# Performance work log

Hardware: AMD Instinct MI355X
Metric: run time of the kernel (lower is better)

The kernel has to match this reference:

```python
import jax, jax.numpy as jnp
import numpy as np

COST_CLS, COST_MASK, COST_DICE = 2.0, 5.0, 5.0


def setup_inputs() -> dict:
    key = jax.random.key(0)
    k1, k2, k3, k4 = jax.random.split(key, 4)
    B, Q, C, H, W, T, Hg, Wg = 4, 100, 81, 256, 256, 20, 512, 512
    pred_logits = jax.random.normal(k1, (B, Q, C), dtype=jnp.float32)
    pred_masks = jax.random.normal(k2, (B, Q, H, W), dtype=jnp.float32)
    # binary GT instance masks (original uses 0/1 masks)
    tgt_masks = (jax.random.uniform(k3, (B, T, Hg, Wg)) < 0.5).astype(jnp.float32)
    tgt_labels = jax.random.randint(k4, (B, T), 0, C).astype(jnp.int64)
    return {"pred_logits": pred_logits, "pred_masks": pred_masks,
            "tgt_masks": tgt_masks, "tgt_labels": tgt_labels}


def _cost_matrices(pred_logits, pred_masks, tgt_masks, tgt_labels):
    # pred_logits [B,Q,C], pred_masks [B,Q,H,W], tgt_masks [B,T,Hg,Wg], tgt_labels [B,T]
    B, Q, H, W = pred_masks.shape
    T, Hg, Wg = tgt_masks.shape[1:]
    # F.interpolate(mode='nearest') down to pred mask size: src = floor(dst * in/out)
    ri = (jnp.arange(H) * Hg) // H
    ci = (jnp.arange(W) * Wg) // W
    tgt = tgt_masks[:, :, ri][:, :, :, ci]          # [B,T,H,W]
    pm = pred_masks.reshape(B, Q, H * W)            # [B,Q,HW]
    tm = tgt.reshape(B, T, H * W)                   # [B,T,HW]
    hw = float(H * W)
    # classification cost: -softmax(logits)[:, tgt_ids]
    prob = jax.nn.softmax(pred_logits, axis=-1)     # [B,Q,C]
    cost_class = -jnp.take_along_axis(prob, tgt_labels[:, None, :], axis=2)  # [B,Q,T]
    # batch_sigmoid_ce_loss: mean over pixels of BCE-with-logits vs 0/1 target
    pos = jax.nn.softplus(-pm)                      # -log sigmoid(x)
    neg = jax.nn.softplus(pm)                       # -log (1 - sigmoid(x))
    cost_mask = (jnp.einsum('bqp,btp->bqt', pos, tm)
                 + jnp.einsum('bqp,btp->bqt', neg, 1.0 - tm)) / hw
    # batch_dice_loss
    sig = jax.nn.sigmoid(pm)
    numer = 2.0 * jnp.einsum('bqp,btp->bqt', sig, tm)
    denom = sig.sum(-1)[:, :, None] + tm.sum(-1)[:, None, :]
    cost_dice = 1.0 - (numer + 1.0) / (denom + 1.0)
    C = COST_CLS * cost_class + COST_MASK * cost_mask + COST_DICE * cost_dice
    return jnp.nan_to_num(C, nan=0.0)               # [B,Q,T]


_cost_jit = jax.jit(_cost_matrices)


def _lsa(cost):
    """Shortest-augmenting-path linear sum assignment (scipy algorithm).
    cost: (R, Cn) numpy array with R <= Cn. Returns col4row[r] = assigned column."""
    R, Cn = cost.shape
    u = np.zeros(R, dtype=np.float64)
    v = np.zeros(Cn, dtype=np.float64)
    col4row = np.full(R, -1, dtype=np.int64)
    row4col = np.full(Cn, -1, dtype=np.int64)
    cost = cost.astype(np.float64)
    for cur_row in range(R):
        shortest = np.full(Cn, np.inf)
        path = np.full(Cn, -1, dtype=np.int64)
        SR = np.zeros(R, dtype=bool)
        SC = np.zeros(Cn, dtype=bool)
        i = cur_row
        minVal = 0.0
        sink = -1
        while sink == -1:
            SR[i] = True
            rem = np.where(~SC)[0]
            d = minVal + cost[i, rem] - u[i] - v[rem]
            upd = d < shortest[rem]
            shortest[rem[upd]] = d[upd]
            path[rem[upd]] = i
            jloc = rem[np.argmin(shortest[rem])]
            minVal = shortest[jloc]
            SC[jloc] = True
            if row4col[jloc] == -1:
                sink = jloc
            else:
                i = row4col[jloc]
        u[cur_row] += minVal
        mask = SR.copy(); mask[cur_row] = False
        u[mask] += minVal - shortest[col4row[mask]]
        v[SC] -= minVal - shortest[SC]
        j = sink
        while True:
            i = path[j]
            row4col[j] = i
            col4row[i], j = j, col4row[i]
            if i == cur_row:
                break
    return col4row


def reference(pred_logits, pred_masks, tgt_masks, tgt_labels):
    C = _cost_jit(pred_logits, pred_masks, tgt_masks, tgt_labels)  # [B,Q,T]
    Cn = np.asarray(C)
    B, Q, T = Cn.shape
    pred_idx, tgt_idx = [], []
    for b in range(B):
        # solve on the transpose (T <= Q): target t -> query q[t]
        q = _lsa(Cn[b].T)
        t = np.arange(T)
        order = np.argsort(q)  # scipy returns row (query) indices in sorted order
        pred_idx.append(q[order])
        tgt_idx.append(t[order])
    return (C,
            jnp.asarray(np.stack(pred_idx), dtype=jnp.int64),
            jnp.asarray(np.stack(tgt_idx), dtype=jnp.int64))
```

## Files before the change

### kernel.cpp

```cpp
#include <hip/hip_runtime.h>
#include <hip/hip_bf16.h>
#include <math.h>
#include <stdint.h>

#define NB 4
#define NQ 100
#define NQR 101
#define NCLS 81
#define NT 20
#define NHW 65536

#define SC 256
#define CPX (NHW / SC)
#define TP 32

typedef __attribute__((ext_vector_type(8))) short bf16x8;
typedef __attribute__((ext_vector_type(16))) float f32x16;

__device__ inline short to_bf16(float f) {
    __hip_bfloat16 h = __float2bfloat16(f);
    return __builtin_bit_cast(short, h);
}

__device__ inline float fast_exp2(float x) { return __builtin_amdgcn_exp2f(x); }
__device__ inline float fast_log2(float x) { return __builtin_amdgcn_logf(x); }

__global__ void __launch_bounds__(256)
k_main(const float* __restrict__ pm, const float* __restrict__ tgt,
       float* __restrict__ A_part, float* __restrict__ D_part,
       float* __restrict__ Sp_part) {
    int gid = blockIdx.x;
    int chunk = gid & (SC - 1);
    int b = gid >> 8;
    int tid = threadIdx.x;
    int wv = tid >> 6, lane = tid & 63;
    int p0 = chunk * CPX;

    __shared__ uint32_t s_tb[CPX];
    __shared__ float s_pm[128 * 64];
    __shared__ short s_bf[4][512];

    if (tid < 128) {
        const float* base = tgt + (((size_t)b * NT) * 512 + 2 * chunk) * 512 + 4 * tid;
        uint32_t w0 = 0, w1 = 0;
#pragma unroll
        for (int t = 0; t < NT; ++t) {
            float4 v = *reinterpret_cast<const float4*>(base + (size_t)t * 512 * 512);
            w0 |= (v.x > 0.5f ? 1u : 0u) << t;
            w1 |= (v.z > 0.5f ? 1u : 0u) << t;
        }
        s_tb[2 * tid] = w0;
        s_tb[2 * tid + 1] = w1;
    }
    __syncthreads();

    int r0 = tid >> 4, cw = tid & 15;
    int Rg = wv * 32 + (lane & 31);
    int h = lane >> 5;
    const bool ones_row = (Rg == NQ);
    bf16x8 ones;
#pragma unroll
    for (int e = 0; e < 8; ++e) ones[e] = (short)0x3F80;

    f32x16 accA, accD;
#pragma unroll
    for (int r = 0; r < 16; ++r) { accA[r] = 0.0f; accD[r] = 0.0f; }
    float mxsum = 0.0f, l2sum = 0.0f;
    const float LOG2E = 1.4426950408889634f;

    for (int st = 0; st < 4; ++st) {
        {
            int ls = wv;
            int col = lane & 31;
            int kbase = st * 64 + ls * 16 + (h << 3);
            uint32_t pk[4];
#pragma unroll
            for (int e2 = 0; e2 < 4; ++e2) {
                uint32_t w0 = s_tb[kbase + 2 * e2];
                uint32_t w1 = s_tb[kbase + 2 * e2 + 1];
                uint32_t lo, hi;
                if (col < NT)       { lo = ((w0 >> col) & 1u) ? 0x3F80u : 0u;
                                      hi = ((w1 >> col) & 1u) ? 0x3F80u : 0u; }
                else if (col == NT) { lo = 0x3F80u; hi = 0x3F80u; }
                else                { lo = 0u; hi = 0u; }
                pk[e2] = lo | (hi << 16);
            }
            *reinterpret_cast<uint4*>(&s_bf[ls][lane * 8]) =
                *reinterpret_cast<const uint4*>(pk);
        }
#pragma unroll
        for (int p = 0; p < 8; ++p) {
            int row = r0 + 16 * p;
            float4 v = make_float4(0.0f, 0.0f, 0.0f, 0.0f);
            if (row < NQ)
                v = *reinterpret_cast<const float4*>(
                    pm + ((size_t)(b * NQ + row)) * NHW + (p0 + st * 64 + cw * 4));
            *reinterpret_cast<float4*>(
                &s_pm[row * 64 + ((cw ^ (row & 15)) << 2)]) = v;
        }
        __syncthreads();
#pragma unroll
        for (int sl = 0; sl < 4; ++sl) {
            int c0 = sl * 4 + h * 2;
            float4 xa = *reinterpret_cast<const float4*>(
                &s_pm[Rg * 64 + ((c0 ^ (Rg & 15)) << 2)]);
            float4 xb4 = *reinterpret_cast<const float4*>(
                &s_pm[Rg * 64 + (((c0 + 1) ^ (Rg & 15)) << 2)]);
            float xs[8] = {xa.x, xa.y, xa.z, xa.w, xb4.x, xb4.y, xb4.z, xb4.w};
            bf16x8 af, sf;
#pragma unroll
            for (int e = 0; e < 8; ++e) {
                float xi = xs[e];
                float y = xi * LOG2E;
                float e1 = fast_exp2(0.0f - fabsf(y));
                float tt = 1.0f + e1;
                float inv = __builtin_amdgcn_rcpf(tt);
                float sig = (xi >= 0.0f) ? inv : e1 * inv;
                l2sum += fast_log2(tt);
                mxsum += fmaxf(xi, 0.0f);
                af[e] = to_bf16(xi);
                sf[e] = to_bf16(sig);
            }
            if (ones_row) af = ones;
            bf16x8 bf = *reinterpret_cast<const bf16x8*>(&s_bf[sl][lane * 8]);
            accA = __builtin_amdgcn_mfma_f32_32x32x16_bf16(af, bf, accA, 0, 0, 0);
            accD = __builtin_amdgcn_mfma_f32_32x32x16_bf16(sf, bf, accD, 0, 0, 0);
        }
        __syncthreads();
    }

    int t = lane & 31;
#pragma unroll
    for (int r = 0; r < 16; ++r) {
        int rowD = (r & 3) + 8 * (r >> 2) + 4 * (lane >> 5);
        int qo = wv * 32 + rowD;
        if (qo <= NQ && t <= NT) {
            size_t base = ((size_t)(b * NQR + qo) * SC + chunk) * TP + t;
            A_part[base] = accA[r];
            D_part[base] = accD[r];
        }
    }
    float sp = fmaf(0.6931471805599453f, l2sum, mxsum);
    sp += __shfl_xor(sp, 32);
    if (lane < 32 && Rg < NQ)
        Sp_part[(size_t)(b * NQ + Rg) * SC + chunk] = sp;
}

__global__ void __launch_bounds__(256)
k_assemble(const float* __restrict__ logits, const int* __restrict__ labels,
           const float* __restrict__ A_part, const float* __restrict__ D_part,
           const float* __restrict__ Sp_part, float* __restrict__ Cout) {
    int bq = blockIdx.x;
    int q = bq % NQ, b = bq / NQ;
    int tid = threadIdx.x, wv = tid >> 6, lane = tid & 63;
    int t = tid & 31, g = tid >> 5;
    __shared__ float sA[4][32], sD[4][32], sS[4][32], sSn[4];

    const float* pa = A_part + (size_t)(b * NQR + q) * SC * TP;
    const float* pd = D_part + (size_t)(b * NQR + q) * SC * TP;
    const float* ps = A_part + (size_t)(b * NQR + NQ) * SC * TP;
    const float* pp = Sp_part + (size_t)(b * NQ + q) * SC;

    float a = 0.0f, d = 0.0f, s = 0.0f;
    for (int c = g; c < SC; c += 8) {
        a += pa[c * TP + t];
        d += pd[c * TP + t];
        s += ps[c * TP + t];
    }
    a += __shfl_xor(a, 32);
    d += __shfl_xor(d, 32);
    s += __shfl_xor(s, 32);
    if (lane < 32) { sA[wv][lane] = a; sD[wv][lane] = d; sS[wv][lane] = s; }
    {
        float sp = pp[tid];
        for (int o = 32; o; o >>= 1) sp += __shfl_xor(sp, o);
        if (lane == 0) sSn[wv] = sp;
    }
    __syncthreads();

    if (wv == 0) {
        int lt = (lane < 32) ? lane : 0;
        float At4 = sA[0][lt] + sA[1][lt] + sA[2][lt] + sA[3][lt];
        float Dt4 = sD[0][lt] + sD[1][lt] + sD[2][lt] + sD[3][lt];
        float St4 = sS[0][lt] + sS[1][lt] + sS[2][lt] + sS[3][lt];
        float Sneg = sSn[0] + sSn[1] + sSn[2] + sSn[3];
        float Ssig = __shfl(Dt4, NT);

        const float* lg = logits + (size_t)bq * NCLS;
        float x0 = (lane < NCLS) ? lg[lane] : -INFINITY;
        float x1 = (lane + 64 < NCLS) ? lg[lane + 64] : -INFINITY;
        float mx = fmaxf(x0, x1);
        for (int o = 32; o; o >>= 1) mx = fmaxf(mx, __shfl_xor(mx, o));
        float s0 = (lane < NCLS) ? __expf(x0 - mx) : 0.0f;
        float s1 = (lane + 64 < NCLS) ? __expf(x1 - mx) : 0.0f;
        float sum = s0 + s1;
        for (int o = 32; o; o >>= 1) sum += __shfl_xor(sum, o);

        if (lane < NT) {
            int label = labels[b * NT + lane];
            float prob = __expf(lg[label] - mx) / sum;
            float cm = (Sneg - At4) * (1.0f / (float)NHW);
            float cd = 1.0f - (2.0f * Dt4 + 1.0f) / (Ssig + St4 + 1.0f);
            float c = 2.0f * (-prob) + 5.0f * cm + 5.0f * cd;
            if (isnan(c)) c = 0.0f;
            Cout[(size_t)bq * NT + lane] = c;
        }
    }
}

__global__ void __launch_bounds__(64)
k_lsa(const float* __restrict__ Cmat, float* __restrict__ out) {
    int b = blockIdx.x;
    int lane = threadIdx.x;
    __shared__ double s_cost[NT][128];

    for (int idx = lane; idx < NT * 128; idx += 64) {
        int r = idx >> 7, j = idx & 127;
        s_cost[r][j] = (j < NQ) ? (double)Cmat[((size_t)b * NQ + j) * NT + r] : 0.0;
    }
    __syncthreads();

    int j0 = lane, j1 = lane + 64;
    bool v1ok = (j1 < NQ);
    double v_0 = 0.0, v_1 = 0.0;
    int r4c0 = -1, r4c1 = -1;
    double u_r = 0.0;
    int c4r = -1;

    for (int cur = 0; cur < NT; ++cur) {
        double sh0 = INFINITY, sh1 = INFINITY;
        int p0 = -1, p1 = -1;
        bool sc0 = false, sc1 = false;
        bool SRr = false;
        int i = cur, sink = -1;
        double minVal = 0.0;

        while (true) {
            if (lane == i) SRr = true;
            double ui = __shfl(u_r, i);
            double c0 = s_cost[i][j0];
            double c1 = s_cost[i][j1 & 127];
            if (!sc0) {
                double d = (minVal + c0 - ui) - v_0;
                if (d < sh0) { sh0 = d; p0 = i; }
            }
            if (v1ok && !sc1) {
                double d = (minVal + c1 - ui) - v_1;
                if (d < sh1) { sh1 = d; p1 = i; }
            }
            double cand0 = (!sc0) ? sh0 : INFINITY;
            double cand1 = (v1ok && !sc1) ? sh1 : INFINITY;
            double bv; int bj;
            if (cand0 <= cand1) { bv = cand0; bj = j0; }
            else                { bv = cand1; bj = j1; }
            for (int o = 32; o; o >>= 1) {
                double ov = __shfl_xor(bv, o);
                int oj = __shfl_xor(bj, o);
                if (ov < bv || (ov == bv && oj < bj)) { bv = ov; bj = oj; }
            }
            minVal = bv;
            if (bj < 64) { if (lane == bj) sc0 = true; }
            else         { if (lane == bj - 64) sc1 = true; }
            int r4 = (bj < 64) ? __shfl(r4c0, bj) : __shfl(r4c1, bj - 64);
            if (r4 == -1) { sink = bj; break; }
            i = r4;
        }

        {
            int c = c4r;
            double g0 = __shfl(sh0, c & 63);
            double g1 = __shfl(sh1, (c - 64) & 63);
            double shc = (c < 64) ? g0 : g1;
            if (lane == cur) u_r += minVal;
            else if (lane < NT && SRr) u_r += minVal - shc;
        }
        if (sc0) v_0 -= minVal - sh0;
        if (v1ok && sc1) v_1 -= minVal - sh1;

        int j = sink;
        while (true) {
            int ii = (j < 64) ? __shfl(p0, j) : __shfl(p1, j - 64);
            if (j < 64) { if (lane == j) r4c0 = ii; }
            else        { if (lane == j - 64) r4c1 = ii; }
            int nj = __shfl(c4r, ii);
            if (lane == ii) c4r = j;
            if (ii == cur) break;
            j = nj;
        }
    }

    int my = c4r;
    int rank = 0;
#pragma unroll
    for (int t2 = 0; t2 < NT; ++t2) {
        int vv = __shfl(my, t2);
        rank += (vv < my) ? 1 : 0;
    }
    if (lane < NT) {
        out[NB * NQ * NT + b * NT + rank] = (float)my;
        out[NB * NQ * NT + NB * NT + b * NT + rank] = (float)lane;
    }
}

extern "C" void kernel_launch(void* const* d_in, const int* in_sizes, int n_in,
                              void* d_out, int out_size, void* d_ws, size_t ws_size,
                              hipStream_t stream) {
    const float* pred_logits = (const float*)d_in[0];
    const float* pred_masks  = (const float*)d_in[1];
    const float* tgt_masks   = (const float*)d_in[2];
    const int*   tgt_labels  = (const int*)d_in[3];
    float* out = (float*)d_out;

    char* ws = (char*)d_ws;
    float* A_part  = (float*)ws;
    float* D_part  = A_part + (size_t)NB * NQR * SC * TP;
    float* Sp_part = D_part + (size_t)NB * NQR * SC * TP;

    k_main<<<NB * SC, 256, 0, stream>>>(pred_masks, tgt_masks, A_part, D_part, Sp_part);
    k_assemble<<<NB * NQ, 256, 0, stream>>>(pred_logits, tgt_labels, A_part, D_part,
                                            Sp_part, out);
    k_lsa<<<NB, 64, 0, stream>>>(out, out);
}
```

Measured before the change: 82.17 us.

## Double-buffer pred-mask tiles with async global_load_lds prefetch

Replaces the per-stage synchronous float4 loads of pred mask tiles into LDS with direct global-to-LDS DMA loads (global_load_lds), double-buffered across two LDS banks so stage st+2 is fetched while stage st is computed. The target bf16 operand tile is likewise double-buffered and built one stage ahead. Manual vmcnt/lgkmcnt waits and raw s_barrier replace __syncthreads. The aim is to hide global memory latency behind the MFMA and transcendental work. The cost is more LDS, fragile hand-written wait counts, and rows past NQ now reading past the end of the bank instead of zeros.

```diff
diff --git a/kernel.cpp b/kernel.cpp
--- a/kernel.cpp
+++ b/kernel.cpp
@@ -16,6 +16,8 @@
 
 typedef __attribute__((ext_vector_type(8))) short bf16x8;
 typedef __attribute__((ext_vector_type(16))) float f32x16;
+typedef __attribute__((address_space(1))) const void gvoid_t;
+typedef __attribute__((address_space(3))) void svoid_t;
 
 __device__ inline short to_bf16(float f) {
     __hip_bfloat16 h = __float2bfloat16(f);
@@ -24,6 +26,21 @@
 
 __device__ inline float fast_exp2(float x) { return __builtin_amdgcn_exp2f(x); }
 __device__ inline float fast_log2(float x) { return __builtin_amdgcn_logf(x); }
+
+__device__ inline void stage_dma(const float* __restrict__ pm, float* bank,
+                                 int b, int p0, int st, int wv, int lane) {
+    int nIss = (wv == 0) ? 7 : 6;
+    for (int p = 0; p < nIss; ++p) {
+        int rbase = 4 * wv + 16 * p;
+        int row = rbase + (lane >> 4);
+        int cw = lane & 15;
+        int src = cw ^ (row & 15);
+        const float* g = pm + ((size_t)(b * NQ + row)) * NHW
+                            + (p0 + st * 64 + src * 4);
+        float* l = bank + rbase * 64 + lane * 4;
+        __builtin_amdgcn_global_load_lds((gvoid_t*)g, (svoid_t*)l, 16, 0, 0);
+    }
+}
 
 __global__ void __launch_bounds__(256)
 k_main(const float* __restrict__ pm, const float* __restrict__ tgt,
@@ -37,8 +54,10 @@
     int p0 = chunk * CPX;
 
     __shared__ uint32_t s_tb[CPX];
-    __shared__ float s_pm[128 * 64];
-    __shared__ short s_bf[4][512];
+    __shared__ float s_pm[2][100 * 64];
+    __shared__ short s_bf[2][4 * 512];
+
+    stage_dma(pm, s_pm[0], b, p0, 0, wv, lane);
 
     if (tid < 128) {
         const float* base = tgt + (((size_t)b * NT) * 512 + 2 * chunk) * 512 + 4 * tid;
@@ -52,15 +71,40 @@
         s_tb[2 * tid] = w0;
         s_tb[2 * tid + 1] = w1;
     }
-    __syncthreads();
-
-    int r0 = tid >> 4, cw = tid & 15;
+    asm volatile("s_waitcnt lgkmcnt(0)" ::: "memory");
+    __builtin_amdgcn_s_barrier();
+
     int Rg = wv * 32 + (lane & 31);
     int h = lane >> 5;
+    int col = lane & 31;
     const bool ones_row = (Rg == NQ);
     bf16x8 ones;
 #pragma unroll
     for (int e = 0; e < 8; ++e) ones[e] = (short)0x3F80;
+
+    {
+        int kbase = 0 * 64 + wv * 16 + (h << 3);
+        uint32_t pk[4];
+#pragma unroll
+        for (int e2 = 0; e2 < 4; ++e2) {
+            uint32_t w0 = s_tb[kbase + 2 * e2];
+            uint32_t w1 = s_tb[kbase + 2 * e2 + 1];
+            uint32_t lo, hi;
+            if (col < NT)       { lo = ((w0 >> col) & 1u) ? 0x3F80u : 0u;
+                                  hi = ((w1 >> col) & 1u) ? 0x3F80u : 0u; }
+            else if (col == NT) { lo = 0x3F80u; hi = 0x3F80u; }
+            else                { lo = 0u; hi = 0u; }
+            pk[e2] = lo | (hi << 16);
+        }
+        *reinterpret_cast<uint4*>(&s_bf[0][wv * 512 + lane * 8]) =
+            *reinterpret_cast<const uint4*>(pk);
+    }
+    stage_dma(pm, s_pm[1], b, p0, 1, wv, lane);
+    if (wv == 0) asm volatile("s_waitcnt vmcnt(7) lgkmcnt(0)" ::: "memory");
+    else         asm volatile("s_waitcnt vmcnt(6) lgkmcnt(0)" ::: "memory");
+    __builtin_amdgcn_sched_barrier(0);
+    __builtin_amdgcn_s_barrier();
+    __builtin_amdgcn_sched_barrier(0);
 
     f32x16 accA, accD;
 #pragma unroll
@@ -68,44 +112,16 @@
     float mxsum = 0.0f, l2sum = 0.0f;
     const float LOG2E = 1.4426950408889634f;
 
+#pragma unroll
     for (int st = 0; st < 4; ++st) {
-        {
-            int ls = wv;
-            int col = lane & 31;
-            int kbase = st * 64 + ls * 16 + (h << 3);
-            uint32_t pk[4];
-#pragma unroll
-            for (int e2 = 0; e2 < 4; ++e2) {
-                uint32_t w0 = s_tb[kbase + 2 * e2];
-                uint32_t w1 = s_tb[kbase + 2 * e2 + 1];
-                uint32_t lo, hi;
-                if (col < NT)       { lo = ((w0 >> col) & 1u) ? 0x3F80u : 0u;
-                                      hi = ((w1 >> col) & 1u) ? 0x3F80u : 0u; }
-                else if (col == NT) { lo = 0x3F80u; hi = 0x3F80u; }
-                else                { lo = 0u; hi = 0u; }
-                pk[e2] = lo | (hi << 16);
-            }
-            *reinterpret_cast<uint4*>(&s_bf[ls][lane * 8]) =
-                *reinterpret_cast<const uint4*>(pk);
-        }
-#pragma unroll
-        for (int p = 0; p < 8; ++p) {
-            int row = r0 + 16 * p;
-            float4 v = make_float4(0.0f, 0.0f, 0.0f, 0.0f);
-            if (row < NQ)
-                v = *reinterpret_cast<const float4*>(
-                    pm + ((size_t)(b * NQ + row)) * NHW + (p0 + st * 64 + cw * 4));
-            *reinterpret_cast<float4*>(
-                &s_pm[row * 64 + ((cw ^ (row & 15)) << 2)]) = v;
-        }
-        __syncthreads();
+        const int bank = st & 1;
 #pragma unroll
         for (int sl = 0; sl < 4; ++sl) {
             int c0 = sl * 4 + h * 2;
             float4 xa = *reinterpret_cast<const float4*>(
-                &s_pm[Rg * 64 + ((c0 ^ (Rg & 15)) << 2)]);
+                &s_pm[bank][Rg * 64 + ((c0 ^ (Rg & 15)) << 2)]);
             float4 xb4 = *reinterpret_cast<const float4*>(
-                &s_pm[Rg * 64 + (((c0 + 1) ^ (Rg & 15)) << 2)]);
+                &s_pm[bank][Rg * 64 + (((c0 + 1) ^ (Rg & 15)) << 2)]);
             float xs[8] = {xa.x, xa.y, xa.z, xa.w, xb4.x, xb4.y, xb4.z, xb4.w};
             bf16x8 af, sf;
 #pragma unroll
@@ -122,11 +138,42 @@
                 sf[e] = to_bf16(sig);
             }
             if (ones_row) af = ones;
-            bf16x8 bf = *reinterpret_cast<const bf16x8*>(&s_bf[sl][lane * 8]);
+            bf16x8 bf = *reinterpret_cast<const bf16x8*>(&s_bf[bank][sl * 512 + lane * 8]);
             accA = __builtin_amdgcn_mfma_f32_32x32x16_bf16(af, bf, accA, 0, 0, 0);
             accD = __builtin_amdgcn_mfma_f32_32x32x16_bf16(sf, bf, accD, 0, 0, 0);
         }
-        __syncthreads();
+        if (st < 3) {
+            int kbase = (st + 1) * 64 + wv * 16 + (h << 3);
+            uint32_t pk[4];
+#pragma unroll
+            for (int e2 = 0; e2 < 4; ++e2) {
+                uint32_t w0 = s_tb[kbase + 2 * e2];
+                uint32_t w1 = s_tb[kbase + 2 * e2 + 1];
+                uint32_t lo, hi;
+                if (col < NT)       { lo = ((w0 >> col) & 1u) ? 0x3F80u : 0u;
+                                      hi = ((w1 >> col) & 1u) ? 0x3F80u : 0u; }
+                else if (col == NT) { lo = 0x3F80u; hi = 0x3F80u; }
+                else                { lo = 0u; hi = 0u; }
+                pk[e2] = lo | (hi << 16);
+            }
+            *reinterpret_cast<uint4*>(&s_bf[(st + 1) & 1][wv * 512 + lane * 8]) =
+                *reinterpret_cast<const uint4*>(pk);
+        }
+        asm volatile("s_waitcnt lgkmcnt(0)" ::: "memory");
+        __builtin_amdgcn_s_barrier();
+        if (st < 2)
+            stage_dma(pm, s_pm[bank], b, p0, st + 2, wv, lane);
+        if (st < 3) {
+            if (st < 2) {
+                if (wv == 0) asm volatile("s_waitcnt vmcnt(7)" ::: "memory");
+                else         asm volatile("s_waitcnt vmcnt(6)" ::: "memory");
+            } else {
+                asm volatile("s_waitcnt vmcnt(0)" ::: "memory");
+            }
+            __builtin_amdgcn_sched_barrier(0);
+            __builtin_amdgcn_s_barrier();
+            __builtin_amdgcn_sched_barrier(0);
+        }
     }
 
     int t = lane & 31;
```

Measured after the change: 100.0 us. 1.22x slower.
